# Optimization experiments

Measured on AMD Instinct MI355X. Metric: run time of the kernel, lower is better.

## Reference

```python
import jax, jax.numpy as jnp
import numpy as np
from jax import lax

EPS = 1e-5  # BatchNorm eps (inference mode)

def _bn(x, g, b, m, v):
    # inference batchnorm over channel axis 1 of NCHW
    s = g / jnp.sqrt(v + EPS)
    return x * s[None, :, None, None] + (b - m * s)[None, :, None, None]

def _conv1x1(w, x):
    # w: [O, C], x: [B, C, H, W]
    return jnp.einsum('oc,bchw->bohw', w, x)

def setup_inputs() -> dict:
    key = jax.random.key(0)
    ks = jax.random.split(key, 40)
    B, Cin, S = 8, 2048, 64
    R, D, H, NC = 128, 512, 64, 19
    f32 = jnp.float32
    def n(k, shape, scale):
        return jax.random.normal(k, shape, dtype=f32) * scale
    inp = {}
    inp['x'] = jax.random.normal(ks[0], (B, Cin, S, S), f32)
    inp['feat_w'] = n(ks[1], (D, Cin, 3, 3), 0.02)
    # 4 batchnorms: feat, encoding, fusion, conv6
    for i, name in enumerate(['bn1', 'bn2', 'bn3', 'bn4']):
        kk = jax.random.split(ks[2 + i], 4)
        inp[name + '_g'] = jax.random.uniform(kk[0], (D,), f32, 0.5, 1.5)
        inp[name + '_b'] = n(kk[1], (D,), 0.05)
        inp[name + '_m'] = n(kk[2], (D,), 0.1)
        inp[name + '_v'] = jax.random.uniform(kk[3], (D,), f32, 0.5, 1.5)
    inp['enc_w'] = n(ks[6], (D, D), 0.05)
    inp['fc_w'] = n(ks[7], (D, D), 0.05)
    inp['fc_b'] = n(ks[8], (D,), 0.05)
    inp['w1'] = n(ks[9], (R, D, D), 0.05)   # conv1_1[i]: 512->512 1x1
    inp['w2'] = n(ks[10], (R, H, H), 0.05)  # conv1_2[i]: 64->64 1x1
    inp['w3'] = n(ks[11], (R, H, H), 0.05)  # conv1_3[i]: 64->64 1x1
    inp['fusion_w'] = n(ks[12], (D, D), 0.05)
    inp['c6a_w'] = n(ks[13], (D, 2 * D), 0.05)
    inp['c6b_w'] = n(ks[14], (NC, D), 0.05)
    inp['c6b_b'] = n(ks[15], (NC,), 0.05)
    return inp

def reference(x, feat_w,
              bn1_g, bn1_b, bn1_m, bn1_v,
              bn2_g, bn2_b, bn2_m, bn2_v,
              bn3_g, bn3_b, bn3_m, bn3_v,
              bn4_g, bn4_b, bn4_m, bn4_v,
              enc_w, fc_w, fc_b, w1, w2, w3,
              fusion_w, c6a_w, c6b_w, c6b_b):
    # self.feat: 3x3 conv -> BN -> ReLU
    feat = jax.nn.relu(_bn(
        lax.conv_general_dilated(x, feat_w, (1, 1), 'SAME',
                                 dimension_numbers=('NCHW', 'OIHW', 'NCHW')),
        bn1_g, bn1_b, bn1_m, bn1_v))

    # EncModule (se_loss=False)
    enc = jax.nn.relu(_bn(_conv1x1(enc_w, feat), bn2_g, bn2_b, bn2_m, bn2_v))
    en = enc.mean(axis=(2, 3))                                # [B, 512]
    gamma = jax.nn.sigmoid(en @ fc_w.T + fc_b)                # [B, 512]
    se_out = jax.nn.relu(feat * (1.0 + gamma[:, :, None, None]))

    # ContextDecomp: pooled mode vectors (AdaptiveAvgPool2d(1) of permutes)
    Cvec = feat.mean(axis=(2, 3))   # [B, 512] channel vector
    Hvec = feat.mean(axis=(1, 2))   # [B, 64]  (avg over channel & height -> width axis)
    Wvec = feat.mean(axis=(1, 3))   # [B, 64]  (avg over channel & width  -> height axis)
    # all 128 rank-wise 1x1 convs + sigmoid, batched over rank r
    CC = jax.nn.sigmoid(jnp.einsum('roc,bc->bro', w1, Cvec))  # [B, R, 512]
    HH = jax.nn.sigmoid(jnp.einsum('roh,bh->bro', w2, Hvec))  # [B, R, 64]
    WW = jax.nn.sigmoid(jnp.einsum('row,bw->bro', w3, Wvec))  # [B, R, 64]
    # Tucker/CP reconstruction summed over ranks; torch layout puts the
    # width-derived vector (HH) on spatial axis 2 and height-derived (WW) on axis 3
    t1 = jnp.einsum('brc,bri,brj->bcij', CC, HH, WW) * 0.015625  # 1/64
    t = feat * (1.0 + t1)
    outs = jax.nn.relu(_bn(_conv1x1(fusion_w, t), bn3_g, bn3_b, bn3_m, bn3_v))

    # conv6 head: cat -> 1x1 conv -> BN -> ReLU -> (dropout eval=id) -> 1x1 conv
    cat = jnp.concatenate([outs, se_out], axis=1)              # [B, 1024, 64, 64]
    h6 = jax.nn.relu(_bn(_conv1x1(c6a_w, cat), bn4_g, bn4_b, bn4_m, bn4_v))
    out = _conv1x1(c6b_w, h6) + c6b_b[None, :, None, None]     # [B, 19, 64, 64]
    return out
```

## Files before the change

### kernel.cpp

```cpp
#include <hip/hip_runtime.h>
#include <stdint.h>
#include <stddef.h>

using u16 = unsigned short;
using u32 = unsigned int;

typedef __attribute__((ext_vector_type(8))) short short8;
typedef __attribute__((ext_vector_type(4))) float f32x4;

#define DEV static __device__ __forceinline__

DEV float bf2f(u16 v){ union{u32 u; float f;} x; x.u = ((u32)v)<<16; return x.f; }
DEV u16 f2bf(float f){ union{float f; u32 u;} x; x.f = f; u32 r = (x.u + 0x7FFFu + ((x.u>>16)&1u))>>16; return (u16)r; }
DEV float lo16(u32 u){ union{u32 u; float f;} x; x.u = u<<16; return x.f; }
DEV float hi16(u32 u){ union{u32 u; float f;} x; x.u = u & 0xFFFF0000u; return x.f; }

DEV void gload16(const u16* g, u16* l){
  __builtin_amdgcn_global_load_lds((const __attribute__((address_space(1))) void*)g,
                                   (__attribute__((address_space(3))) void*)l, 16, 0, 0);
}

#define BAR    __builtin_amdgcn_s_barrier()
#define SCHED0 __builtin_amdgcn_sched_barrier(0)
#define PRIO1  __builtin_amdgcn_s_setprio(1)
#define PRIO0  __builtin_amdgcn_s_setprio(0)
#define VMC4   asm volatile("s_waitcnt vmcnt(4)" ::: "memory")
#define VMC0   asm volatile("s_waitcnt vmcnt(0)" ::: "memory")

__global__ __launch_bounds__(512, 2)
void conv_gemm256(const u16* __restrict__ xp, const u16* __restrict__ wt,
                  u16* __restrict__ O, const float* __restrict__ sb,
                  float* __restrict__ Cvec, float* __restrict__ Hvec,
                  float* __restrict__ Wvec)
{
  constexpr int NT = 288;
  __shared__ u16 smA[2*256*64];
  __shared__ u16 smB[2*256*64];
  const int t = threadIdx.x;
  const int lane = t & 63;
  const int wv = t >> 6;
  const int wr = wv >> 2, wc = wv & 3;
  const int mt = blockIdx.x, nt = blockIdx.y, b = blockIdx.z;
  const int ij0 = mt*256, n0 = nt*256;
  const u16* Ab = xp + (size_t)b*66*66*2048;

  const int tA   = t >> 3;
  const int sc8  = ((t&7) ^ ((t>>3)&7)) * 8;
  const int ldsc = (t&7) * 8;
  const int qB   = t >> 8;
  const int rB   = (t>>3) & 31;

  f32x4 acc[8][4];
  #pragma unroll
  for (int i=0;i<8;++i)
    #pragma unroll
    for (int j=0;j<4;++j) acc[i][j] = (f32x4){0.f,0.f,0.f,0.f};

  short8 aR[4][2];
  short8 bR[2][2][2];

#define STG_A(dst, s, kt_) do{ \
    const int ktc = (kt_) < NT ? (kt_) : (NT-1); \
    const int tap = ktc>>5; const int ty = (tap*11)>>5; const int tx = tap - ty*3; \
    const size_t ko = ((size_t)(ktc&31))<<6; \
    _Pragma("unroll") for (int l=0;l<2;++l){ \
      const int row = (s)*64 + tA + l*128; \
      const u16* src = Ab + ((size_t)((mt*4 + (s) + l*2 + ty)*66 + tA + tx))*2048 + ko + sc8; \
      gload16(src, (dst) + row*64 + ldsc); } }while(0)

#define STG_B(dst, s, kt_) do{ \
    const int ktc = (kt_) < NT ? (kt_) : (NT-1); \
    const int tap = ktc>>5; \
    const size_t ko = (size_t)tap*2048 + (((size_t)(ktc&31))<<6); \
    _Pragma("unroll") for (int l=0;l<2;++l){ \
      const int row = (l*2 + qB)*64 + (s)*32 + rB; \
      const u16* src = wt + ((size_t)(n0 + row))*9*2048 + ko + sc8; \
      gload16(src, (dst) + row*64 + ldsc); } }while(0)

#define LDA_(base, mh) do{ _Pragma("unroll") for(int mi=0;mi<4;++mi){ \
    const int r = wr*128 + (mh)*64 + mi*16 + (lane&15); \
    _Pragma("unroll") for(int kk=0;kk<2;++kk){ \
      const int ch = (kk*4 + (lane>>4)) ^ (r&7); \
      aR[mi][kk] = *(const short8*)&(base)[r*64 + ch*8]; } } }while(0)
#define LDB_(base, nh) do{ _Pragma("unroll") for(int ni=0;ni<2;++ni){ \
    const int r = wc*64 + (nh)*32 + ni*16 + (lane&15); \
    _Pragma("unroll") for(int kk=0;kk<2;++kk){ \
      const int ch = (kk*4 + (lane>>4)) ^ (r&7); \
      bR[nh][ni][kk] = *(const short8*)&(base)[r*64 + ch*8]; } } }while(0)
#define MFMAQ(mh, nh) do{ _Pragma("unroll") for(int mi=0;mi<4;++mi) \
    _Pragma("unroll") for(int ni=0;ni<2;++ni){ \
      acc[(mh)*4+mi][(nh)*2+ni] = __builtin_amdgcn_mfma_f32_16x16x32_bf16(aR[mi][0], bR[nh][ni][0], acc[(mh)*4+mi][(nh)*2+ni],0,0,0); \
      acc[(mh)*4+mi][(nh)*2+ni] = __builtin_amdgcn_mfma_f32_16x16x32_bf16(aR[mi][1], bR[nh][ni][1], acc[(mh)*4+mi][(nh)*2+ni],0,0,0); } }while(0)

  STG_A(smA, 0, 0);
  STG_B(smB, 0, 0);
  STG_B(smB, 1, 0);
  STG_A(smA, 1, 0);
  VMC4;
  BAR; SCHED0;

  for (int j=0; j<NT; ++j) {
    const int p = j & 1;
    const u16* As = smA + (p<<14);
    const u16* Bs = smB + (p<<14);
    u16* Aalt = smA + ((p^1)<<14);
    u16* Balt = smB + ((p^1)<<14);

    LDA_(As, 0); LDB_(Bs, 0);
    STG_A(Aalt, 0, j+1);
    BAR; SCHED0;
    PRIO1; MFMAQ(0,0); PRIO0;
    VMC4;
    BAR; SCHED0;

    LDB_(Bs, 1);
    STG_B(Balt, 0, j+1);
    BAR; SCHED0;
    PRIO1; MFMAQ(0,1); PRIO0;
    VMC4;
    BAR; SCHED0;

    LDA_(As, 1);
    STG_B(Balt, 1, j+1);
    BAR; SCHED0;
    PRIO1; MFMAQ(1,0); PRIO0;
    BAR; SCHED0;

    STG_A(Aalt, 1, j+1);
    BAR; SCHED0;
    PRIO1; MFMAQ(1,1); PRIO0;
    VMC4;
    BAR; SCHED0;
  }

  VMC0;
  BAR;
  float* red = (float*)smA;
  if (t < 324) red[t] = 0.f;
  BAR;

  float xs[4][4];
  #pragma unroll
  for (int q=0;q<4;++q)
    #pragma unroll
    for (int j2=0;j2<4;++j2) xs[q][j2] = 0.f;
  float ys0 = 0.f, ys1 = 0.f;

  #pragma unroll
  for (int n=0; n<4; ++n) {
    const int cloc = wc*64 + (n>>1)*32 + (n&1)*16 + (lane&15);
    const int col = n0 + cloc;
    const float s = sb[col], bb = sb[512+col];
    float cs = 0.f;
    #pragma unroll
    for (int a=0; a<8; ++a) {
      const int row0 = ij0 + wr*128 + (a>>2)*64 + (a&3)*16 + ((lane>>4)<<2);
      #pragma unroll
      for (int j2=0; j2<4; ++j2) {
        const size_t idx = ((size_t)(b*4096 + row0 + j2))*512 + col;
        float v = acc[a][n][j2]*s + bb;
        v = v > 0.f ? v : 0.f;
        O[idx] = f2bf(v);
        cs += v;
        xs[a&3][j2] += v;
        if (a < 4) ys0 += v; else ys1 += v;
      }
    }
    atomicAdd(&red[cloc], cs);
  }
  #pragma unroll
  for (int off=1; off<16; off<<=1)
    #pragma unroll
    for (int q=0;q<4;++q)
      #pragma unroll
      for (int j2=0;j2<4;++j2) xs[q][j2] += __shfl_xor(xs[q][j2], off);
  if ((lane & 15) == 0) {
    #pragma unroll
    for (int q=0;q<4;++q)
      #pragma unroll
      for (int j2=0;j2<4;++j2)
        atomicAdd(&red[256 + q*16 + (lane>>4)*4 + j2], xs[q][j2]);
  }
  #pragma unroll
  for (int off=1; off<64; off<<=1) { ys0 += __shfl_xor(ys0, off); ys1 += __shfl_xor(ys1, off); }
  if (lane == 0) {
    atomicAdd(&red[320 + wr*2 + 0], ys0);
    atomicAdd(&red[320 + wr*2 + 1], ys1);
  }
  BAR;
  if (t < 256)       atomicAdd(&Cvec[b*512 + n0 + t], red[t]*(1.0f/4096.0f));
  else if (t < 320)  atomicAdd(&Hvec[b*64 + (t-256)], red[t]*(1.0f/32768.0f));
  else if (t < 324)  atomicAdd(&Wvec[b*64 + (ij0>>6) + (t-320)], red[t]*(1.0f/32768.0f));
#undef STG_A
#undef STG_B
#undef LDA_
#undef LDB_
#undef MFMAQ
}

template<int V>
__global__ __launch_bounds__(256)
void gemm128(const u16* __restrict__ A, const u16* __restrict__ Bw, u16* __restrict__ O,
             const u16* __restrict__ feat, const u16* __restrict__ B2,
             const float* __restrict__ sb, float* __restrict__ en)
{
  constexpr int NSEG = (V==4)?2:1;
  constexpr int KSEG = (V==2)?128:512;
  __shared__ u16 smA[128*64];
  __shared__ u16 smB[128*64];
  const int tid = threadIdx.x;
  const int lane = tid & 63;
  const int wv = tid >> 6;
  const int wr = wv >> 1, wc = wv & 1;
  const int mt = blockIdx.x, nt = blockIdx.y, b = blockIdx.z;
  const int ij0 = mt*128, n0 = nt*128;
  const int srow = tid >> 3, schunk = tid & 7;

  f32x4 acc[4][4];
  #pragma unroll
  for (int i=0;i<4;++i)
    #pragma unroll
    for (int j=0;j<4;++j) acc[i][j] = (f32x4){0.f,0.f,0.f,0.f};

  for (int seg=0; seg<NSEG; ++seg) {
    const u16* Ab;
    const u16* Bb;
    if constexpr (V==1 || V==3) { Ab = A + (size_t)b*4096*512; Bb = Bw; }
    else if constexpr (V==2) { Ab = A + (size_t)b*4096*128; Bb = Bw + (size_t)b*512*128; }
    else { Ab = (seg==0 ? A : feat) + (size_t)b*4096*512;
           Bb = (seg==0) ? Bw : (B2 + (size_t)b*512*512); }

    for (int kt=0; kt<KSEG/64; ++kt) {
      const int k0 = kt*64;
      #pragma unroll
      for (int i=0;i<4;++i) {
        const int row = i*32 + srow;
        const int sc = schunk ^ (row & 7);
        const u16* src;
        if constexpr (V==2) src = Ab + (size_t)(ij0+row)*128 + (k0 + sc*8);
        else                src = Ab + (size_t)(ij0+row)*512 + (k0 + sc*8);
        gload16(src, &smA[row*64 + schunk*8]);
      }
      #pragma unroll
      for (int i=0;i<4;++i) {
        const int row = i*32 + srow;
        const int sc = schunk ^ (row & 7);
        const int o = n0 + row;
        const u16* src;
        if constexpr (V==2) src = Bb + (size_t)o*128 + (k0 + sc*8);
        else                src = Bb + (size_t)o*512 + (k0 + sc*8);
        gload16(src, &smB[row*64 + schunk*8]);
      }
      __syncthreads();
      #pragma unroll
      for (int ks=0; ks<2; ++ks) {
        short8 av[4], bv[4];
        #pragma unroll
        for (int mi=0;mi<4;++mi) {
          const int r = wr*64 + mi*16 + (lane & 15);
          const int ch = (ks*4 + (lane>>4)) ^ (r & 7);
          av[mi] = *(const short8*)&smA[r*64 + ch*8];
        }
        #pragma unroll
        for (int ni=0;ni<4;++ni) {
          const int r = wc*64 + ni*16 + (lane & 15);
          const int ch = (ks*4 + (lane>>4)) ^ (r & 7);
          bv[ni] = *(const short8*)&smB[r*64 + ch*8];
        }
        #pragma unroll
        for (int mi=0;mi<4;++mi)
          #pragma unroll
          for (int ni=0;ni<4;++ni)
            acc[mi][ni] = __builtin_amdgcn_mfma_f32_16x16x32_bf16(av[mi], bv[ni], acc[mi][ni], 0, 0, 0);
      }
      __syncthreads();
    }
  }

  if constexpr (V==1) {
    #pragma unroll
    for (int ni=0;ni<4;++ni) {
      const int col = n0 + wc*64 + ni*16 + (lane & 15);
      const float s = sb[col], bb = sb[512+col];
      float cs = 0.f;
      #pragma unroll
      for (int mi=0;mi<4;++mi)
        #pragma unroll
        for (int j=0;j<4;++j) {
          float v = acc[mi][ni][j]*s + bb;
          cs += (v > 0.f) ? v : 0.f;
        }
      cs += __shfl_xor(cs, 16);
      cs += __shfl_xor(cs, 32);
      if (lane < 16) atomicAdd(&en[b*512 + col], cs * (1.0f/4096.0f));
    }
  } else {
    #pragma unroll
    for (int ni=0;ni<4;++ni) {
      const int col = n0 + wc*64 + ni*16 + (lane & 15);
      float s = 0.f, bb = 0.f;
      if constexpr (V!=2) { s = sb[col]; bb = sb[512+col]; }
      #pragma unroll
      for (int mi=0;mi<4;++mi) {
        const int row0 = ij0 + wr*64 + mi*16 + ((lane>>4)<<2);
        #pragma unroll
        for (int j=0;j<4;++j) {
          const size_t idx = ((size_t)(b*4096 + row0 + j))*512 + col;
          float v = acc[mi][ni][j];
          if constexpr (V==2) {
            O[idx] = f2bf(bf2f(feat[idx]) * (1.0f + v));
          } else {
            v = v*s + bb;
            O[idx] = f2bf(v > 0.f ? v : 0.f);
          }
        }
      }
    }
  }
}

__global__ __launch_bounds__(256)
void prep_weights(const float* __restrict__ fw, const float* __restrict__ encw,
                  const float* __restrict__ fusw, const float* __restrict__ c6aw,
                  const float* g1,const float* b1,const float* m1,const float* v1,
                  const float* g2,const float* b2,const float* m2,const float* v2,
                  const float* g3,const float* b3,const float* m3,const float* v3,
                  const float* g4,const float* b4,const float* m4,const float* v4,
                  u16* __restrict__ wt, u16* __restrict__ encb,
                  u16* __restrict__ fusb, u16* __restrict__ c6a1,
                  float* __restrict__ bnsb)
{
  const int bx = blockIdx.x, t = threadIdx.x;
  if (bx < 512) {
    const int o = bx;
    for (int c = t; c < 2048; c += 256) {
      const float* src = fw + ((size_t)o*2048 + c)*9;
      #pragma unroll
      for (int tt=0; tt<9; ++tt)
        wt[((size_t)o*9 + tt)*2048 + c] = f2bf(src[tt]);
    }
  } else if (bx < 1536) {
    const int i = (bx-512)*256 + t;
    encb[i] = f2bf(encw[i]);
  } else if (bx < 2560) {
    const int i = (bx-1536)*256 + t;
    fusb[i] = f2bf(fusw[i]);
  } else if (bx < 3584) {
    const int i = (bx-2560)*256 + t;
    c6a1[i] = f2bf(c6aw[(size_t)(i>>9)*1024 + (i&511)]);
  } else {
    const int c = (bx-3584)*256 + t;
    if (c < 512) {
      const float eps = 1e-5f;
      float s1 = g1[c]*rsqrtf(v1[c]+eps); bnsb[c]      = s1; bnsb[512+c]  = b1[c]-m1[c]*s1;
      float s2 = g2[c]*rsqrtf(v2[c]+eps); bnsb[1024+c] = s2; bnsb[1536+c] = b2[c]-m2[c]*s2;
      float s3 = g3[c]*rsqrtf(v3[c]+eps); bnsb[2048+c] = s3; bnsb[2560+c] = b3[c]-m3[c]*s3;
      float s4 = g4[c]*rsqrtf(v4[c]+eps); bnsb[3072+c] = s4; bnsb[3584+c] = b4[c]-m4[c]*s4;
    }
  }
}

__global__ __launch_bounds__(256)
void pad_x(const float* __restrict__ x, u16* __restrict__ xp)
{
  __shared__ u16 tile[256*66];
  const int bx = blockIdx.x;
  const int cb = bx & 7, y = (bx>>3) & 63, b = bx >> 9;
  const int t = threadIdx.x;
  const int xcol = t & 63, crow = t >> 6;
  for (int it=0; it<64; ++it) {
    const int cl = it*4 + crow;
    tile[cl*66 + xcol] = f2bf(x[(((size_t)b*2048 + cb*256 + cl)*64 + y)*64 + xcol]);
  }
  __syncthreads();
  const size_t rowbase = (size_t)(b*66 + y + 1)*66;
  for (int px=0; px<64; ++px)
    xp[(rowbase + px + 1)*2048 + cb*256 + t] = tile[t*66 + px];
  xp[rowbase*2048 + cb*256 + t] = 0;
  xp[(rowbase + 65)*2048 + cb*256 + t] = 0;
  if (y == 0) {
    const size_t rb = (size_t)(b*66)*66;
    for (int px=0; px<66; ++px) xp[(rb+px)*2048 + cb*256 + t] = 0;
  }
  if (y == 63) {
    const size_t rb = (size_t)(b*66 + 65)*66;
    for (int px=0; px<66; ++px) xp[(rb+px)*2048 + cb*256 + t] = 0;
  }
}

__global__ __launch_bounds__(256)
void small1(const float* __restrict__ en, const float* __restrict__ fcw, const float* __restrict__ fcb,
            const float* __restrict__ w1, const float* __restrict__ Cvec,
            const float* __restrict__ w2, const float* __restrict__ w3,
            const float* __restrict__ Hvec, const float* __restrict__ Wvec,
            float* __restrict__ gamma, u16* __restrict__ CCT,
            float* __restrict__ HH, float* __restrict__ WW)
{
  const int bx = blockIdx.x, t = threadIdx.x;
  if (bx < 8) {
    __shared__ float enl[512];
    const int b = bx;
    for (int c=t;c<512;c+=256) enl[c] = en[b*512+c];
    __syncthreads();
    for (int o=t;o<512;o+=256) {
      float a = fcb[o];
      const float* wr = fcw + (size_t)o*512;
      for (int c=0;c<512;++c) a += enl[c]*wr[c];
      gamma[b*512+o] = 1.0f/(1.0f+__expf(-a));
    }
  } else if (bx < 136) {
    __shared__ float hl[512], wl[512];
    const int r = bx - 8;
    for (int i=t;i<512;i+=256){ hl[i]=Hvec[i]; wl[i]=Wvec[i]; }
    __syncthreads();
    const int i = t & 63, bh = t >> 6;
    for (int bb=bh; bb<8; bb+=4) {
      float sh=0.f, sw=0.f;
      const float* w2r = w2 + ((size_t)r*64 + i)*64;
      const float* w3r = w3 + ((size_t)r*64 + i)*64;
      #pragma unroll 8
      for (int h=0;h<64;++h){ sh += w2r[h]*hl[bb*64+h]; sw += w3r[h]*wl[bb*64+h]; }
      HH[((size_t)bb*128 + r)*64 + i] = 1.0f/(1.0f+__expf(-sh));
      WW[((size_t)bb*128 + r)*64 + i] = 1.0f/(1.0f+__expf(-sw));
    }
  } else {
    __shared__ float cv[4096];
    for (int i=t;i<4096;i+=256) cv[i] = Cvec[i];
    __syncthreads();
    const int p = (bx-136)*4 + (t>>6);
    const int r = p >> 9, o = p & 511;
    const int lane = t & 63;
    float ab[8] = {0,0,0,0,0,0,0,0};
    const float* w1r = w1 + ((size_t)r*512 + o)*512;
    #pragma unroll
    for (int it=0; it<8; ++it) {
      const float wvv = w1r[it*64 + lane];
      #pragma unroll
      for (int bb=0;bb<8;++bb) ab[bb] += wvv * cv[bb*512 + it*64 + lane];
    }
    #pragma unroll
    for (int off=32; off; off>>=1)
      #pragma unroll
      for (int bb=0;bb<8;++bb) ab[bb] += __shfl_xor(ab[bb], off);
    #pragma unroll
    for (int bb=0;bb<8;++bb)
      if (lane == bb)
        CCT[((size_t)bb*512 + o)*128 + r] = f2bf((1.0f/(1.0f+__expf(-ab[bb]))) * 0.015625f);
  }
}

__global__ __launch_bounds__(256)
void small2(const float* __restrict__ c6aw, const float* __restrict__ gamma,
            const float* __restrict__ HH, const float* __restrict__ WW,
            u16* __restrict__ w2b, u16* __restrict__ HWT)
{
  const int bx = blockIdx.x, t = threadIdx.x;
  if (bx < 4096) {
    const int b = bx >> 9, o = bx & 511;
    const float* src = c6aw + (size_t)o*1024 + 512;
    const float* gmv = gamma + b*512;
    u16* dst = w2b + ((size_t)b*512 + o)*512;
    for (int c=t;c<512;c+=256) dst[c] = f2bf(src[c]*(1.0f+gmv[c]));
  } else {
    __shared__ float wwl[64*129];
    __shared__ float hhy[128];
    const int idx = bx - 4096;
    const int b = idx >> 6, y = idx & 63;
    for (int g=t; g<8192; g+=256){ const int r=g>>6, xx=g&63; wwl[xx*129+r] = WW[((size_t)b*128+r)*64+xx]; }
    if (t < 128) hhy[t] = HH[((size_t)b*128 + t)*64 + y];
    __syncthreads();
    const int r2 = (t & 63)*2, xg = t >> 6;
    for (int xx=xg; xx<64; xx+=4) {
      const float v0 = hhy[r2]   * wwl[xx*129 + r2];
      const float v1 = hhy[r2+1] * wwl[xx*129 + r2 + 1];
      const u32 pk = (u32)f2bf(v0) | ((u32)f2bf(v1)<<16);
      *(u32*)&HWT[((size_t)(b*4096 + y*64 + xx))*128 + r2] = pk;
    }
  }
}

__global__ __launch_bounds__(256)
void c6b_head(const u16* __restrict__ h6, const float* __restrict__ w,
              const float* __restrict__ bias, float* __restrict__ out)
{
  const int gid = blockIdx.x*256 + threadIdx.x;
  const int b = gid >> 12, ij = gid & 4095;
  float acc[19];
  #pragma unroll
  for (int o=0;o<19;++o) acc[o] = bias[o];
  const u16* hp = h6 + (size_t)gid*512;
  for (int c0=0;c0<512;c0+=8) {
    const uint4 d = *(const uint4*)(hp + c0);
    const float f0=lo16(d.x),f1=hi16(d.x),f2=lo16(d.y),f3=hi16(d.y),
                f4=lo16(d.z),f5=hi16(d.z),f6=lo16(d.w),f7=hi16(d.w);
    #pragma unroll
    for (int o=0;o<19;++o) {
      const float* wr = w + o*512 + c0;
      acc[o] += f0*wr[0] + f1*wr[1] + f2*wr[2] + f3*wr[3]
              + f4*wr[4] + f5*wr[5] + f6*wr[6] + f7*wr[7];
    }
  }
  #pragma unroll
  for (int o=0;o<19;++o) out[((size_t)(b*19 + o))*4096 + ij] = acc[o];
}

extern "C" void kernel_launch(void* const* d_in, const int* in_sizes, int n_in,
                              void* d_out, int out_size, void* d_ws, size_t ws_size,
                              hipStream_t stream)
{
  (void)in_sizes; (void)n_in; (void)out_size;
  const float* x     = (const float*)d_in[0];
  const float* fw    = (const float*)d_in[1];
  const float* bnp[16];
  for (int i=0;i<16;++i) bnp[i] = (const float*)d_in[2+i];
  const float* enc_w = (const float*)d_in[18];
  const float* fc_w  = (const float*)d_in[19];
  const float* fc_b  = (const float*)d_in[20];
  const float* w1    = (const float*)d_in[21];
  const float* w2    = (const float*)d_in[22];
  const float* w3    = (const float*)d_in[23];
  const float* fus_w = (const float*)d_in[24];
  const float* c6a_w = (const float*)d_in[25];
  const float* c6b_w = (const float*)d_in[26];
  const float* c6b_b = (const float*)d_in[27];

  char* ws = (char*)d_ws;
  constexpr size_t OFF_XP=0, OFF_T=0, OFF_OUTS=33554432ull, OFF_H6=67108864ull,
    OFF_WT=142737408ull, OFF_FEAT=161611776ull, OFF_HWT=195166208ull, OFF_W2B=203554816ull,
    OFF_CCT=207749120ull, OFF_ENCB=208797696ull, OFF_FUSB=209321984ull, OFF_C6A1=209846272ull,
    OFF_HH=210370560ull, OFF_WW=210632704ull, OFF_EN=210894848ull, OFF_CV=210911232ull,
    OFF_HV=210927616ull, OFF_WV=210929664ull, OFF_GAMMA=210931712ull, OFF_BNSB=210948096ull,
    NEEDED=210964480ull;
  if (ws_size < NEEDED) return;

  u16* xp    = (u16*)(ws + OFF_XP);
  u16* tb    = (u16*)(ws + OFF_T);
  u16* outs  = (u16*)(ws + OFF_OUTS);
  u16* h6    = (u16*)(ws + OFF_H6);
  u16* wt    = (u16*)(ws + OFF_WT);
  u16* featb = (u16*)(ws + OFF_FEAT);
  u16* hwt   = (u16*)(ws + OFF_HWT);
  u16* w2b   = (u16*)(ws + OFF_W2B);
  u16* cct   = (u16*)(ws + OFF_CCT);
  u16* encb  = (u16*)(ws + OFF_ENCB);
  u16* fusb  = (u16*)(ws + OFF_FUSB);
  u16* c6a1  = (u16*)(ws + OFF_C6A1);
  float* HH  = (float*)(ws + OFF_HH);
  float* WW  = (float*)(ws + OFF_WW);
  float* en  = (float*)(ws + OFF_EN);
  float* Cv  = (float*)(ws + OFF_CV);
  float* Hv  = (float*)(ws + OFF_HV);
  float* Wv  = (float*)(ws + OFF_WV);
  float* gm  = (float*)(ws + OFF_GAMMA);
  float* bnsb= (float*)(ws + OFF_BNSB);

  hipMemsetAsync(ws + OFF_EN, 0, 36864, stream);

  prep_weights<<<3586,256,0,stream>>>(fw, enc_w, fus_w, c6a_w,
      bnp[0],bnp[1],bnp[2],bnp[3], bnp[4],bnp[5],bnp[6],bnp[7],
      bnp[8],bnp[9],bnp[10],bnp[11], bnp[12],bnp[13],bnp[14],bnp[15],
      wt, encb, fusb, c6a1, bnsb);
  pad_x<<<4096,256,0,stream>>>(x, xp);
  conv_gemm256<<<dim3(16,2,8),512,0,stream>>>(xp, wt, featb, bnsb, Cv, Hv, Wv);
  gemm128<1><<<dim3(32,4,8),256,0,stream>>>(featb, encb, nullptr, nullptr, nullptr, bnsb+1024, en);
  small1<<<16520,256,0,stream>>>(en, fc_w, fc_b, w1, Cv, w2, w3, Hv, Wv, gm, cct, HH, WW);
  small2<<<4608,256,0,stream>>>(c6a_w, gm, HH, WW, w2b, hwt);
  gemm128<2><<<dim3(32,4,8),256,0,stream>>>(hwt, cct, tb, featb, nullptr, nullptr, nullptr);
  gemm128<3><<<dim3(32,4,8),256,0,stream>>>(tb, fusb, outs, nullptr, nullptr, bnsb+2048, nullptr);
  gemm128<4><<<dim3(32,4,8),256,0,stream>>>(outs, c6a1, h6, featb, w2b, bnsb+3072, nullptr);
  c6b_head<<<128,256,0,stream>>>(h6, c6b_w, c6b_b, (float*)d_out);
}
```

Baseline: 965.0 us.

## Replace 128-tile 1x1 GEMMs with double-buffered 256x256 pipelined GEMM kernel

Adds a gemm256 kernel with 256x256 output tiles, 512 threads, and double-buffered LDS. Global-to-LDS staging for the next k-tile is interleaved with MFMA quarters, using barriers and priority hints. The enc, fusion and conv6a 1x1 convolutions now use this kernel, while gemm128 is reduced to the rank-128 Tucker reconstruction only. The larger tiles and overlapped loads aim for more data reuse and hidden memory latency. In exchange the grid shrinks to 256 blocks, and register pressure and LDS use grow.

```diff
diff --git a/kernel.cpp b/kernel.cpp
--- a/kernel.cpp
+++ b/kernel.cpp
@@ -199,13 +199,164 @@
 }
 
 template<int V>
+__global__ __launch_bounds__(512, 2)
+void gemm256(const u16* __restrict__ A0, const u16* __restrict__ A1,
+             const u16* __restrict__ Bw0, const u16* __restrict__ Bw1,
+             u16* __restrict__ O, const float* __restrict__ sb,
+             float* __restrict__ en)
+{
+  constexpr int NTALL = (V==4) ? 16 : 8;
+  __shared__ u16 smA[2*256*64];
+  __shared__ u16 smB[2*256*64];
+  const int t = threadIdx.x;
+  const int lane = t & 63;
+  const int wv = t >> 6;
+  const int wr = wv >> 2, wc = wv & 3;
+  const int mt = blockIdx.x, nt = blockIdx.y, b = blockIdx.z;
+  const int ij0 = mt*256, n0 = nt*256;
+  const u16* A0b = A0 + (size_t)b*4096*512;
+  const u16* A1b = (V==4) ? (A1 + (size_t)b*4096*512) : nullptr;
+  const u16* B1b = (V==4) ? (Bw1 + (size_t)b*512*512) : nullptr;
+
+  const int tA   = t >> 3;
+  const int sc8  = ((t&7) ^ ((t>>3)&7)) * 8;
+  const int ldsc = (t&7) * 8;
+  const int qB   = t >> 8;
+  const int rB   = (t>>3) & 31;
+
+  f32x4 acc[8][4];
+  #pragma unroll
+  for (int i=0;i<8;++i)
+    #pragma unroll
+    for (int j=0;j<4;++j) acc[i][j] = (f32x4){0.f,0.f,0.f,0.f};
+
+  short8 aR[4][2];
+  short8 bR[2][2][2];
+
+#define STG_A(dst, s, kt_) do{ \
+    const int ktc = (kt_) < NTALL ? (kt_) : (NTALL-1); \
+    const u16* Abase = (V==4 && ktc>=8) ? A1b : A0b; \
+    const size_t ko = ((size_t)(ktc&7))<<6; \
+    _Pragma("unroll") for (int l=0;l<2;++l){ \
+      const int row = (s)*64 + tA + l*128; \
+      const u16* src = Abase + (size_t)(ij0 + row)*512 + ko + sc8; \
+      gload16(src, (dst) + row*64 + ldsc); } }while(0)
+
+#define STG_B(dst, s, kt_) do{ \
+    const int ktc = (kt_) < NTALL ? (kt_) : (NTALL-1); \
+    const u16* Bbase = (V==4 && ktc>=8) ? B1b : Bw0; \
+    const size_t ko = ((size_t)(ktc&7))<<6; \
+    _Pragma("unroll") for (int l=0;l<2;++l){ \
+      const int row = (l*2 + qB)*64 + (s)*32 + rB; \
+      const u16* src = Bbase + (size_t)(n0 + row)*512 + ko + sc8; \
+      gload16(src, (dst) + row*64 + ldsc); } }while(0)
+
+#define LDA_(base, mh) do{ _Pragma("unroll") for(int mi=0;mi<4;++mi){ \
+    const int r = wr*128 + (mh)*64 + mi*16 + (lane&15); \
+    _Pragma("unroll") for(int kk=0;kk<2;++kk){ \
+      const int ch = (kk*4 + (lane>>4)) ^ (r&7); \
+      aR[mi][kk] = *(const short8*)&(base)[r*64 + ch*8]; } } }while(0)
+#define LDB_(base, nh) do{ _Pragma("unroll") for(int ni=0;ni<2;++ni){ \
+    const int r = wc*64 + (nh)*32 + ni*16 + (lane&15); \
+    _Pragma("unroll") for(int kk=0;kk<2;++kk){ \
+      const int ch = (kk*4 + (lane>>4)) ^ (r&7); \
+      bR[nh][ni][kk] = *(const short8*)&(base)[r*64 + ch*8]; } } }while(0)
+#define MFMAQ(mh, nh) do{ _Pragma("unroll") for(int mi=0;mi<4;++mi) \
+    _Pragma("unroll") for(int ni=0;ni<2;++ni){ \
+      acc[(mh)*4+mi][(nh)*2+ni] = __builtin_amdgcn_mfma_f32_16x16x32_bf16(aR[mi][0], bR[nh][ni][0], acc[(mh)*4+mi][(nh)*2+ni],0,0,0); \
+      acc[(mh)*4+mi][(nh)*2+ni] = __builtin_amdgcn_mfma_f32_16x16x32_bf16(aR[mi][1], bR[nh][ni][1], acc[(mh)*4+mi][(nh)*2+ni],0,0,0); } }while(0)
+
+  STG_A(smA, 0, 0);
+  STG_B(smB, 0, 0);
+  STG_B(smB, 1, 0);
+  STG_A(smA, 1, 0);
+  VMC4;
+  BAR; SCHED0;
+
+  for (int j=0; j<NTALL; ++j) {
+    const int p = j & 1;
+    const u16* As = smA + (p<<14);
+    const u16* Bs = smB + (p<<14);
+    u16* Aalt = smA + ((p^1)<<14);
+    u16* Balt = smB + ((p^1)<<14);
+
+    LDA_(As, 0); LDB_(Bs, 0);
+    STG_A(Aalt, 0, j+1);
+    BAR; SCHED0;
+    PRIO1; MFMAQ(0,0); PRIO0;
+    VMC4;
+    BAR; SCHED0;
+
+    LDB_(Bs, 1);
+    STG_B(Balt, 0, j+1);
+    BAR; SCHED0;
+    PRIO1; MFMAQ(0,1); PRIO0;
+    VMC4;
+    BAR; SCHED0;
+
+    LDA_(As, 1);
+    STG_B(Balt, 1, j+1);
+    BAR; SCHED0;
+    PRIO1; MFMAQ(1,0); PRIO0;
+    BAR; SCHED0;
+
+    STG_A(Aalt, 1, j+1);
+    BAR; SCHED0;
+    PRIO1; MFMAQ(1,1); PRIO0;
+    VMC4;
+    BAR; SCHED0;
+  }
+  VMC0;
+
+  if constexpr (V==1) {
+    #pragma unroll
+    for (int n=0; n<4; ++n) {
+      const int col = n0 + wc*64 + (n>>1)*32 + (n&1)*16 + (lane&15);
+      const float s = sb[col], bb = sb[512+col];
+      float cs = 0.f;
+      #pragma unroll
+      for (int a=0; a<8; ++a) {
+        #pragma unroll
+        for (int j2=0; j2<4; ++j2) {
+          float v = acc[a][n][j2]*s + bb;
+          cs += (v > 0.f) ? v : 0.f;
+        }
+      }
+      cs += __shfl_xor(cs, 16);
+      cs += __shfl_xor(cs, 32);
+      if (lane < 16) atomicAdd(&en[b*512 + col], cs * (1.0f/4096.0f));
+    }
+  } else {
+    #pragma unroll
+    for (int n=0; n<4; ++n) {
+      const int col = n0 + wc*64 + (n>>1)*32 + (n&1)*16 + (lane&15);
+      const float s = sb[col], bb = sb[512+col];
+      #pragma unroll
+      for (int a=0; a<8; ++a) {
+        const int row0 = ij0 + wr*128 + (a>>2)*64 + (a&3)*16 + ((lane>>4)<<2);
+        #pragma unroll
+        for (int j2=0; j2<4; ++j2) {
+          const size_t idx = ((size_t)(b*4096 + row0 + j2))*512 + col;
+          float v = acc[a][n][j2]*s + bb;
+          O[idx] = f2bf(v > 0.f ? v : 0.f);
+        }
+      }
+    }
+  }
+#undef STG_A
+#undef STG_B
+#undef LDA_
+#undef LDB_
+#undef MFMAQ
+}
+
+template<int V>
 __global__ __launch_bounds__(256)
 void gemm128(const u16* __restrict__ A, const u16* __restrict__ Bw, u16* __restrict__ O,
              const u16* __restrict__ feat, const u16* __restrict__ B2,
              const float* __restrict__ sb, float* __restrict__ en)
 {
-  constexpr int NSEG = (V==4)?2:1;
-  constexpr int KSEG = (V==2)?128:512;
+  constexpr int KSEG = 128;
   __shared__ u16 smA[128*64];
   __shared__ u16 smB[128*64];
   const int tid = threadIdx.x;
@@ -222,98 +373,58 @@
     #pragma unroll
     for (int j=0;j<4;++j) acc[i][j] = (f32x4){0.f,0.f,0.f,0.f};
 
-  for (int seg=0; seg<NSEG; ++seg) {
-    const u16* Ab;
-    const u16* Bb;
-    if constexpr (V==1 || V==3) { Ab = A + (size_t)b*4096*512; Bb = Bw; }
-    else if constexpr (V==2) { Ab = A + (size_t)b*4096*128; Bb = Bw + (size_t)b*512*128; }
-    else { Ab = (seg==0 ? A : feat) + (size_t)b*4096*512;
-           Bb = (seg==0) ? Bw : (B2 + (size_t)b*512*512); }
-
-    for (int kt=0; kt<KSEG/64; ++kt) {
-      const int k0 = kt*64;
-      #pragma unroll
-      for (int i=0;i<4;++i) {
-        const int row = i*32 + srow;
-        const int sc = schunk ^ (row & 7);
-        const u16* src;
-        if constexpr (V==2) src = Ab + (size_t)(ij0+row)*128 + (k0 + sc*8);
-        else                src = Ab + (size_t)(ij0+row)*512 + (k0 + sc*8);
-        gload16(src, &smA[row*64 + schunk*8]);
+  const u16* Ab = A + (size_t)b*4096*128;
+  const u16* Bb = Bw + (size_t)b*512*128;
+
+  for (int kt=0; kt<KSEG/64; ++kt) {
+    const int k0 = kt*64;
+    #pragma unroll
+    for (int i=0;i<4;++i) {
+      const int row = i*32 + srow;
+      const int sc = schunk ^ (row & 7);
+      gload16(Ab + (size_t)(ij0+row)*128 + (k0 + sc*8), &smA[row*64 + schunk*8]);
+    }
+    #pragma unroll
+    for (int i=0;i<4;++i) {
+      const int row = i*32 + srow;
+      const int sc = schunk ^ (row & 7);
+      gload16(Bb + (size_t)(n0+row)*128 + (k0 + sc*8), &smB[row*64 + schunk*8]);
+    }
+    __syncthreads();
+    #pragma unroll
+    for (int ks=0; ks<2; ++ks) {
+      short8 av[4], bv[4];
+      #pragma unroll
+      for (int mi=0;mi<4;++mi) {
+        const int r = wr*64 + mi*16 + (lane & 15);
+        const int ch = (ks*4 + (lane>>4)) ^ (r & 7);
+        av[mi] = *(const short8*)&smA[r*64 + ch*8];
       }
       #pragma unroll
-      for (int i=0;i<4;++i) {
-        const int row = i*32 + srow;
-        const int sc = schunk ^ (row & 7);
-        const int o = n0 + row;
-        const u16* src;
-        if constexpr (V==2) src = Bb + (size_t)o*128 + (k0 + sc*8);
-        else                src = Bb + (size_t)o*512 + (k0 + sc*8);
-        gload16(src, &smB[row*64 + schunk*8]);
+      for (int ni=0;ni<4;++ni) {
+        const int r = wc*64 + ni*16 + (lane & 15);
+        const int ch = (ks*4 + (lane>>4)) ^ (r & 7);
+        bv[ni] = *(const short8*)&smB[r*64 + ch*8];
       }
-      __syncthreads();
-      #pragma unroll
-      for (int ks=0; ks<2; ++ks) {
-        short8 av[4], bv[4];
-        #pragma unroll
-        for (int mi=0;mi<4;++mi) {
-          const int r = wr*64 + mi*16 + (lane & 15);
-          const int ch = (ks*4 + (lane>>4)) ^ (r & 7);
-          av[mi] = *(const short8*)&smA[r*64 + ch*8];
-        }
-        #pragma unroll
-        for (int ni=0;ni<4;++ni) {
-          const int r = wc*64 + ni*16 + (lane & 15);
-          const int ch = (ks*4 + (lane>>4)) ^ (r & 7);
-          bv[ni] = *(const short8*)&smB[r*64 + ch*8];
-        }
-        #pragma unroll
-        for (int mi=0;mi<4;++mi)
-          #pragma unroll
-          for (int ni=0;ni<4;++ni)
-            acc[mi][ni] = __builtin_amdgcn_mfma_f32_16x16x32_bf16(av[mi], bv[ni], acc[mi][ni], 0, 0, 0);
-      }
-      __syncthreads();
-    }
-  }
-
-  if constexpr (V==1) {
-    #pragma unroll
-    for (int ni=0;ni<4;++ni) {
-      const int col = n0 + wc*64 + ni*16 + (lane & 15);
-      const float s = sb[col], bb = sb[512+col];
-      float cs = 0.f;
       #pragma unroll
       for (int mi=0;mi<4;++mi)
         #pragma unroll
-        for (int j=0;j<4;++j) {
-          float v = acc[mi][ni][j]*s + bb;
-          cs += (v > 0.f) ? v : 0.f;
-        }
-      cs += __shfl_xor(cs, 16);
-      cs += __shfl_xor(cs, 32);
-      if (lane < 16) atomicAdd(&en[b*512 + col], cs * (1.0f/4096.0f));
-    }
-  } else {
-    #pragma unroll
-    for (int ni=0;ni<4;++ni) {
-      const int col = n0 + wc*64 + ni*16 + (lane & 15);
-      float s = 0.f, bb = 0.f;
-      if constexpr (V!=2) { s = sb[col]; bb = sb[512+col]; }
-      #pragma unroll
-      for (int mi=0;mi<4;++mi) {
-        const int row0 = ij0 + wr*64 + mi*16 + ((lane>>4)<<2);
-        #pragma unroll
-        for (int j=0;j<4;++j) {
-          const size_t idx = ((size_t)(b*4096 + row0 + j))*512 + col;
-          float v = acc[mi][ni][j];
-          if constexpr (V==2) {
-            O[idx] = f2bf(bf2f(feat[idx]) * (1.0f + v));
-          } else {
-            v = v*s + bb;
-            O[idx] = f2bf(v > 0.f ? v : 0.f);
-          }
-        }
+        for (int ni=0;ni<4;++ni)
+          acc[mi][ni] = __builtin_amdgcn_mfma_f32_16x16x32_bf16(av[mi], bv[ni], acc[mi][ni], 0, 0, 0);
+    }
+    __syncthreads();
+  }
+
+  #pragma unroll
+  for (int ni=0;ni<4;++ni) {
+    const int col = n0 + wc*64 + ni*16 + (lane & 15);
+    #pragma unroll
+    for (int mi=0;mi<4;++mi) {
+      const int row0 = ij0 + wr*64 + mi*16 + ((lane>>4)<<2);
+      #pragma unroll
+      for (int j=0;j<4;++j) {
+        const size_t idx = ((size_t)(b*4096 + row0 + j))*512 + col;
+        O[idx] = f2bf(bf2f(feat[idx]) * (1.0f + acc[mi][ni][j]));
       }
     }
   }
@@ -562,11 +673,11 @@
       wt, encb, fusb, c6a1, bnsb);
   pad_x<<<4096,256,0,stream>>>(x, xp);
   conv_gemm256<<<dim3(16,2,8),512,0,stream>>>(xp, wt, featb, bnsb, Cv, Hv, Wv);
-  gemm128<1><<<dim3(32,4,8),256,0,stream>>>(featb, encb, nullptr, nullptr, nullptr, bnsb+1024, en);
+  gemm256<1><<<dim3(16,2,8),512,0,stream>>>(featb, nullptr, encb, nullptr, nullptr, bnsb+1024, en);
   small1<<<16520,256,0,stream>>>(en, fc_w, fc_b, w1, Cv, w2, w3, Hv, Wv, gm, cct, HH, WW);
   small2<<<4608,256,0,stream>>>(c6a_w, gm, HH, WW, w2b, hwt);
   gemm128<2><<<dim3(32,4,8),256,0,stream>>>(hwt, cct, tb, featb, nullptr, nullptr, nullptr);
-  gemm128<3><<<dim3(32,4,8),256,0,stream>>>(tb, fusb, outs, nullptr, nullptr, bnsb+2048, nullptr);
-  gemm128<4><<<dim3(32,4,8),256,0,stream>>>(outs, c6a1, h6, featb, w2b, bnsb+3072, nullptr);
+  gemm256<3><<<dim3(16,2,8),512,0,stream>>>(tb, nullptr, fusb, nullptr, outs, bnsb+2048, nullptr);
+  gemm256<4><<<dim3(16,2,8),512,0,stream>>>(outs, featb, c6a1, w2b, h6, bnsb+3072, nullptr);
   c6b_head<<<128,256,0,stream>>>(h6, c6b_w, c6b_b, (float*)d_out);
 }
```

Measured after the change: 953.7 us. No clear change (-1.2%).
